# Performance work log

Hardware: AMD Instinct MI355X
Metric: run time of the kernel (lower is better)

Reference implementation:

```python
import jax, jax.numpy as jnp
import numpy as np

N_NODES = 100000
N_EDGES = 1600000
NFEAT = 64
NHID = 64
NCLASS = 40


def setup_inputs() -> dict:
    key = jax.random.key(0)
    ks = jax.random.split(key, 8)
    x = jax.random.normal(ks[0], (N_NODES, NFEAT), dtype=jnp.float32)
    edge_index = jax.random.randint(ks[1], (2, N_EDGES), 0, N_NODES, dtype=jnp.int64)
    # Kaiming-ish small init for Linear weights (stored as [in, out])
    def lin(k, fan_in, fan_out):
        bound = 1.0 / np.sqrt(fan_in)
        kw, kb = jax.random.split(k)
        W = jax.random.uniform(kw, (fan_in, fan_out), jnp.float32, -bound, bound)
        b = jax.random.uniform(kb, (fan_out,), jnp.float32, -bound, bound)
        return W, b
    W1, b1 = lin(ks[2], NFEAT, NHID)
    W2, b2 = lin(ks[3], NHID, NHID)
    Wf, bf = lin(ks[4], NHID, NCLASS)
    return {"x": x, "edge_index": edge_index, "W1": W1, "b1": b1,
            "W2": W2, "b2": b2, "Wf": Wf, "bf": bf}


def _gin_conv(h, src, dst, W, b, n_nodes):
    # PyG GINConv, eps=0: nn(x + sum_{j in N(i)} x_j), nn = Linear -> ReLU
    msg = h[src]                                   # [E, d] gather
    agg = jax.ops.segment_sum(msg, dst, num_segments=n_nodes)  # [N, d] scatter-add
    return jax.nn.relu((h + agg) @ W + b)


def reference(x, edge_index, W1, b1, W2, b2, Wf, bf):
    src, dst = edge_index[0], edge_index[1]
    n = x.shape[0]
    # layer 1: outer F.relu is idempotent on the ReLU inside GINConv's nn
    h = jax.nn.relu(_gin_conv(x, src, dst, W1, b1, n))
    # dropout is identity in eval mode
    h = jax.nn.relu(_gin_conv(h, src, dst, W2, b2, n))
    logits = h @ Wf + bf
    return jax.nn.log_softmax(logits, axis=1)
```

## Files before the change

### kernel.cpp

```cpp
#include <hip/hip_runtime.h>
#include <math.h>

#define N_NODES 100000
#define N_EDGES 1600000
#define NFEAT 64
#define NCLASS 40

#define SCAN_CHUNK 1024
#define SCAN_BLOCKS ((N_NODES + SCAN_CHUNK - 1) / SCAN_CHUNK)

#define NRANGES 8
#define RSZ ((N_NODES + NRANGES - 1) / NRANGES)
#define FILL_SLOTS 64

__device__ __forceinline__ float bf2f(unsigned short u) {
  return __uint_as_float(((unsigned int)u) << 16);
}
__device__ __forceinline__ unsigned short f2bf(float f) {
  unsigned int u = __float_as_uint(f);
  u += 0x7FFFu + ((u >> 16) & 1u);
  return (unsigned short)(u >> 16);
}

__global__ __launch_bounds__(256) void hist_rank_cvt_k(
    const int* __restrict__ dst, int* __restrict__ deg,
    unsigned short* __restrict__ rank, const float* __restrict__ x,
    unsigned short* __restrict__ xb) {
  int e = blockIdx.x * 256 + threadIdx.x;
  if (e < N_EDGES) {
    rank[e] = (unsigned short)atomicAdd(&deg[dst[e]], 1);
    float4 v = reinterpret_cast<const float4*>(x)[e];
    ushort4 o;
    o.x = f2bf(v.x); o.y = f2bf(v.y); o.z = f2bf(v.z); o.w = f2bf(v.w);
    reinterpret_cast<ushort4*>(xb)[e] = o;
  }
}

__global__ __launch_bounds__(256) void scan_partial_k(
    const int* __restrict__ deg, int* __restrict__ blockSums) {
  __shared__ int red[256];
  int b = blockIdx.x, t = threadIdx.x;
  int base = b * SCAN_CHUNK;
  int s = 0;
  for (int i = t; i < SCAN_CHUNK; i += 256) {
    int idx = base + i;
    if (idx < N_NODES) s += deg[idx];
  }
  red[t] = s;
  __syncthreads();
  for (int off = 128; off; off >>= 1) {
    if (t < off) red[t] += red[t + off];
    __syncthreads();
  }
  if (t == 0) blockSums[b] = red[0];
}

__global__ __launch_bounds__(128) void scan_sums_k(int* __restrict__ blockSums,
                                                   int* __restrict__ offs) {
  __shared__ int part[128];
  int t = threadIdx.x;
  int v = (t < SCAN_BLOCKS) ? blockSums[t] : 0;
  part[t] = v;
  __syncthreads();
  for (int off = 1; off < 128; off <<= 1) {
    int add = (t >= off) ? part[t - off] : 0;
    __syncthreads();
    part[t] += add;
    __syncthreads();
  }
  if (t < SCAN_BLOCKS) blockSums[t] = (t == 0) ? 0 : part[t - 1];
  if (t == 127) offs[N_NODES] = part[127];
}

__global__ __launch_bounds__(256) void scan_final_k(
    const int* __restrict__ deg, const int* __restrict__ blockOffs,
    int* __restrict__ offs) {
  __shared__ int part[256];
  int b = blockIdx.x, t = threadIdx.x;
  int base = b * SCAN_CHUNK + t * 4;
  int v0 = 0, v1 = 0, v2 = 0, v3 = 0;
  if (base + 3 < N_NODES) {
    v0 = deg[base]; v1 = deg[base + 1]; v2 = deg[base + 2]; v3 = deg[base + 3];
  } else {
    if (base + 0 < N_NODES) v0 = deg[base + 0];
    if (base + 1 < N_NODES) v1 = deg[base + 1];
    if (base + 2 < N_NODES) v2 = deg[base + 2];
    if (base + 3 < N_NODES) v3 = deg[base + 3];
  }
  part[t] = v0 + v1 + v2 + v3;
  __syncthreads();
  for (int off = 1; off < 256; off <<= 1) {
    int add = (t >= off) ? part[t - off] : 0;
    __syncthreads();
    part[t] += add;
    __syncthreads();
  }
  int run = blockOffs[b] + ((t == 0) ? 0 : part[t - 1]);
  if (base + 0 < N_NODES) { offs[base + 0] = run; run += v0; }
  if (base + 1 < N_NODES) { offs[base + 1] = run; run += v1; }
  if (base + 2 < N_NODES) { offs[base + 2] = run; run += v2; }
  if (base + 3 < N_NODES) { offs[base + 3] = run; run += v3; }
}

__global__ __launch_bounds__(256) void fill_csr_xcd_k(
    const int* __restrict__ src, const int* __restrict__ dst,
    const unsigned short* __restrict__ rank, const int* __restrict__ offs,
    int* __restrict__ csr) {
  const int NQ = N_EDGES / 4;
  int range = blockIdx.x & (NRANGES - 1);
  int slot = blockIdx.x >> 3;
  unsigned int lo = range * RSZ;

  for (int q = slot * 256 + threadIdx.x; q < NQ; q += FILL_SLOTS * 256) {
    int e = q << 2;
    int4 s = *reinterpret_cast<const int4*>(src + e);
    int4 d = *reinterpret_cast<const int4*>(dst + e);
    ushort4 r = *reinterpret_cast<const ushort4*>(rank + e);
    if ((unsigned int)(d.x - lo) < (unsigned int)RSZ) csr[offs[d.x] + r.x] = s.x;
    if ((unsigned int)(d.y - lo) < (unsigned int)RSZ) csr[offs[d.y] + r.y] = s.y;
    if ((unsigned int)(d.z - lo) < (unsigned int)RSZ) csr[offs[d.z] + r.z] = s.z;
    if ((unsigned int)(d.w - lo) < (unsigned int)RSZ) csr[offs[d.w] + r.w] = s.w;
  }
}

__global__ __launch_bounds__(256) void gather_b_k(
    const unsigned short* __restrict__ hb, const int* __restrict__ offs,
    const int* __restrict__ csr, unsigned short* __restrict__ aggb) {
  int t = threadIdx.x;
  int wv = t >> 6;
  int lane = t & 63;
  int g = lane >> 4;
  int l = lane & 15;
  int node = blockIdx.x * 4 + wv;
  if (node >= N_NODES) return;

  int beg = offs[node], end = offs[node + 1];
  float a0 = 0.f, a1 = 0.f, a2 = 0.f, a3 = 0.f;
  int e = beg + g;
  for (; e + 4 < end; e += 8) {
    int s0 = csr[e];
    int s1 = csr[e + 4];
    ushort4 u0 = *reinterpret_cast<const ushort4*>(hb + (size_t)s0 * NFEAT + (l << 2));
    ushort4 u1 = *reinterpret_cast<const ushort4*>(hb + (size_t)s1 * NFEAT + (l << 2));
    a0 += bf2f(u0.x) + bf2f(u1.x);
    a1 += bf2f(u0.y) + bf2f(u1.y);
    a2 += bf2f(u0.z) + bf2f(u1.z);
    a3 += bf2f(u0.w) + bf2f(u1.w);
  }
  if (e < end) {
    int s = csr[e];
    ushort4 u = *reinterpret_cast<const ushort4*>(hb + (size_t)s * NFEAT + (l << 2));
    a0 += bf2f(u.x); a1 += bf2f(u.y); a2 += bf2f(u.z); a3 += bf2f(u.w);
  }
  a0 += __shfl_xor(a0, 16); a1 += __shfl_xor(a1, 16);
  a2 += __shfl_xor(a2, 16); a3 += __shfl_xor(a3, 16);
  a0 += __shfl_xor(a0, 32); a1 += __shfl_xor(a1, 32);
  a2 += __shfl_xor(a2, 32); a3 += __shfl_xor(a3, 32);

  if (g == 0) {
    ushort4 u = *reinterpret_cast<const ushort4*>(hb + (size_t)node * NFEAT + (l << 2));
    ushort4 o;
    o.x = f2bf(a0 + bf2f(u.x)); o.y = f2bf(a1 + bf2f(u.y));
    o.z = f2bf(a2 + bf2f(u.z)); o.w = f2bf(a3 + bf2f(u.w));
    *reinterpret_cast<ushort4*>(aggb + (size_t)node * NFEAT + (l << 2)) = o;
  }
}

__global__ __launch_bounds__(256) void linear_relu_b_k(
    const unsigned short* __restrict__ inb, const float* __restrict__ W,
    const float* __restrict__ b, unsigned short* __restrict__ outb) {
  __shared__ float sIn[32][68];
  __shared__ float sWT[64][68];
  int r0 = blockIdx.x * 32;
  int t = threadIdx.x;
  for (int i = t; i < 64 * 64; i += 256) {
    int k = i >> 6, c = i & 63;
    sWT[c][k] = W[i];
  }
  for (int i = t; i < 512; i += 256) {
    int r = i >> 4, q = i & 15;
    ushort4 u = *reinterpret_cast<const ushort4*>(
        inb + (size_t)(r0 + r) * NFEAT + (q << 2));
    float4 v;
    v.x = bf2f(u.x); v.y = bf2f(u.y); v.z = bf2f(u.z); v.w = bf2f(u.w);
    *reinterpret_cast<float4*>(&sIn[r][q << 2]) = v;
  }
  __syncthreads();

  int c = t & 63;
  int rb = t >> 6;
  float acc[8];
#pragma unroll
  for (int i = 0; i < 8; ++i) acc[i] = 0.f;
#pragma unroll
  for (int kq = 0; kq < 16; ++kq) {
    float4 w = *reinterpret_cast<const float4*>(&sWT[c][kq << 2]);
#pragma unroll
    for (int i = 0; i < 8; ++i) {
      float4 v = *reinterpret_cast<const float4*>(&sIn[rb * 8 + i][kq << 2]);
      acc[i] = fmaf(v.x, w.x, fmaf(v.y, w.y, fmaf(v.z, w.z, fmaf(v.w, w.w, acc[i]))));
    }
  }
  float bias = b[c];
#pragma unroll
  for (int i = 0; i < 8; ++i) {
    int gr = r0 + rb * 8 + i;
    outb[(size_t)gr * NFEAT + c] = f2bf(fmaxf(acc[i] + bias, 0.f));
  }
}

__global__ __launch_bounds__(256) void fused_l2_final_k(
    const unsigned short* __restrict__ inb, const float* __restrict__ W2,
    const float* __restrict__ b2, const float* __restrict__ Wf,
    const float* __restrict__ bf, float* __restrict__ out) {
  __shared__ float sIn[32][68];
  __shared__ float sWT[64][68];
  __shared__ float sWfT[NCLASS][68];
  __shared__ float sH[32][68];
  __shared__ float sLse[32];
  float (*sLg)[41] = reinterpret_cast<float(*)[41]>(&sIn[0][0]);

  int r0 = blockIdx.x * 32;
  int t = threadIdx.x;
  int c = t & 63;
  int rb = t >> 6;

  for (int i = t; i < 64 * 64; i += 256) {
    int k = i >> 6, cc = i & 63;
    sWT[cc][k] = W2[i];
  }
  for (int i = t; i < 64 * NCLASS; i += 256) {
    int k = i / NCLASS, cc = i - k * NCLASS;
    sWfT[cc][k] = Wf[i];
  }
  for (int i = t; i < 512; i += 256) {
    int r = i >> 4, q = i & 15;
    ushort4 u = *reinterpret_cast<const ushort4*>(
        inb + (size_t)(r0 + r) * NFEAT + (q << 2));
    float4 v;
    v.x = bf2f(u.x); v.y = bf2f(u.y); v.z = bf2f(u.z); v.w = bf2f(u.w);
    *reinterpret_cast<float4*>(&sIn[r][q << 2]) = v;
  }
  __syncthreads();

  float acc[8];
#pragma unroll
  for (int i = 0; i < 8; ++i) acc[i] = 0.f;
#pragma unroll
  for (int kq = 0; kq < 16; ++kq) {
    float4 w = *reinterpret_cast<const float4*>(&sWT[c][kq << 2]);
#pragma unroll
    for (int i = 0; i < 8; ++i) {
      float4 v = *reinterpret_cast<const float4*>(&sIn[rb * 8 + i][kq << 2]);
      acc[i] = fmaf(v.x, w.x, fmaf(v.y, w.y, fmaf(v.z, w.z, fmaf(v.w, w.w, acc[i]))));
    }
  }
  float bias = b2[c];
#pragma unroll
  for (int i = 0; i < 8; ++i)
    sH[rb * 8 + i][c] = fmaxf(acc[i] + bias, 0.f);
  __syncthreads();

  if (c < NCLASS) {
    float lg[8];
    float bfc = bf[c];
#pragma unroll
    for (int i = 0; i < 8; ++i) lg[i] = bfc;
#pragma unroll
    for (int kq = 0; kq < 16; ++kq) {
      float4 w = *reinterpret_cast<const float4*>(&sWfT[c][kq << 2]);
#pragma unroll
      for (int i = 0; i < 8; ++i) {
        float4 v = *reinterpret_cast<const float4*>(&sH[rb * 8 + i][kq << 2]);
        lg[i] = fmaf(v.x, w.x, fmaf(v.y, w.y, fmaf(v.z, w.z, fmaf(v.w, w.w, lg[i]))));
      }
    }
#pragma unroll
    for (int i = 0; i < 8; ++i) sLg[rb * 8 + i][c] = lg[i];
  }
  __syncthreads();

  if (t < 32) {
    float m = -INFINITY;
#pragma unroll
    for (int j = 0; j < NCLASS; ++j) m = fmaxf(m, sLg[t][j]);
    float s = 0.f;
#pragma unroll
    for (int j = 0; j < NCLASS; ++j) s += expf(sLg[t][j] - m);
    sLse[t] = m + logf(s);
  }
  __syncthreads();

  for (int i = t; i < 32 * NCLASS; i += 256) {
    int r = i / NCLASS, cc = i - r * NCLASS;
    out[(size_t)(r0 + r) * NCLASS + cc] = sLg[r][cc] - sLse[r];
  }
}

extern "C" void kernel_launch(void* const* d_in, const int* in_sizes, int n_in,
                              void* d_out, int out_size, void* d_ws, size_t ws_size,
                              hipStream_t stream) {
  const float* x  = (const float*)d_in[0];
  const int*   ei = (const int*)d_in[1];
  const float* W1 = (const float*)d_in[2];
  const float* b1 = (const float*)d_in[3];
  const float* W2 = (const float*)d_in[4];
  const float* b2 = (const float*)d_in[5];
  const float* Wf = (const float*)d_in[6];
  const float* bf = (const float*)d_in[7];
  float* out = (float*)d_out;

  const int* src = ei;
  const int* dst = ei + N_EDGES;

  const size_t featElems = (size_t)N_NODES * NFEAT;
  unsigned short* xb   = (unsigned short*)d_ws;
  unsigned short* h1b  = xb + featElems;
  unsigned short* aggA = h1b + featElems;
  unsigned short* aggC = aggA + featElems;
  unsigned short* rank = aggC + featElems;
  int* deg       = (int*)(rank + N_EDGES);
  int* offs      = deg + N_NODES;
  int* blockSums = offs + N_NODES + 1;
  int* csr       = blockSums + 128;

  const int edgeBlocks   = (N_EDGES + 255) / 256;
  const int gatherBlocks = (N_NODES + 3) / 4;
  const int linBlocks    = (N_NODES + 31) / 32;

  hipMemsetAsync(deg, 0, N_NODES * sizeof(int), stream);
  hist_rank_cvt_k<<<edgeBlocks, 256, 0, stream>>>(dst, deg, rank, x, xb);
  scan_partial_k<<<SCAN_BLOCKS, 256, 0, stream>>>(deg, blockSums);
  scan_sums_k<<<1, 128, 0, stream>>>(blockSums, offs);
  scan_final_k<<<SCAN_BLOCKS, 256, 0, stream>>>(deg, blockSums, offs);
  fill_csr_xcd_k<<<NRANGES * FILL_SLOTS, 256, 0, stream>>>(src, dst, rank, offs, csr);

  gather_b_k<<<gatherBlocks, 256, 0, stream>>>(xb, offs, csr, aggA);
  linear_relu_b_k<<<linBlocks, 256, 0, stream>>>(aggA, W1, b1, h1b);

  gather_b_k<<<gatherBlocks, 256, 0, stream>>>(h1b, offs, csr, aggC);
  fused_l2_final_k<<<linBlocks, 256, 0, stream>>>(aggC, W2, b2, Wf, bf, out);
}
```

Baseline: 371.5 us.

## Split degree histogram into 8 sub-counters per node and unroll gather by four

Edge counting now spreads atomics over 8 sub-counters per destination node, selected by edge index mod 8, to reduce contention on same-address atomicAdds. The scan kernels read the 8 sub-counts and emit per-sub-bucket base offsets, which the CSR fill uses for placement. The gather loop is also unrolled to four neighbors in flight per lane group. In exchange the counter array and memset grow eightfold, the scan and fill read more data, and an extra base8 array is written.

```diff
diff --git a/kernel.cpp b/kernel.cpp
--- a/kernel.cpp
+++ b/kernel.cpp
@@ -23,12 +23,13 @@
 }
 
 __global__ __launch_bounds__(256) void hist_rank_cvt_k(
-    const int* __restrict__ dst, int* __restrict__ deg,
-    unsigned short* __restrict__ rank, const float* __restrict__ x,
+    const int* __restrict__ dst, int* __restrict__ cnt8,
+    unsigned short* __restrict__ subrank, const float* __restrict__ x,
     unsigned short* __restrict__ xb) {
   int e = blockIdx.x * 256 + threadIdx.x;
   if (e < N_EDGES) {
-    rank[e] = (unsigned short)atomicAdd(&deg[dst[e]], 1);
+    int d = dst[e];
+    subrank[e] = (unsigned short)atomicAdd(&cnt8[(d << 3) | (e & 7)], 1);
     float4 v = reinterpret_cast<const float4*>(x)[e];
     ushort4 o;
     o.x = f2bf(v.x); o.y = f2bf(v.y); o.z = f2bf(v.z); o.w = f2bf(v.w);
@@ -37,14 +38,18 @@
 }
 
 __global__ __launch_bounds__(256) void scan_partial_k(
-    const int* __restrict__ deg, int* __restrict__ blockSums) {
+    const int* __restrict__ cnt8, int* __restrict__ blockSums) {
   __shared__ int red[256];
   int b = blockIdx.x, t = threadIdx.x;
   int base = b * SCAN_CHUNK;
   int s = 0;
   for (int i = t; i < SCAN_CHUNK; i += 256) {
     int idx = base + i;
-    if (idx < N_NODES) s += deg[idx];
+    if (idx < N_NODES) {
+      const int4* p = reinterpret_cast<const int4*>(cnt8 + ((size_t)idx << 3));
+      int4 a = p[0], c = p[1];
+      s += a.x + a.y + a.z + a.w + c.x + c.y + c.z + c.w;
+    }
   }
   red[t] = s;
   __syncthreads();
@@ -73,21 +78,27 @@
 }
 
 __global__ __launch_bounds__(256) void scan_final_k(
-    const int* __restrict__ deg, const int* __restrict__ blockOffs,
-    int* __restrict__ offs) {
+    const int* __restrict__ cnt8, const int* __restrict__ blockOffs,
+    int* __restrict__ offs, int* __restrict__ base8) {
   __shared__ int part[256];
   int b = blockIdx.x, t = threadIdx.x;
   int base = b * SCAN_CHUNK + t * 4;
-  int v0 = 0, v1 = 0, v2 = 0, v3 = 0;
-  if (base + 3 < N_NODES) {
-    v0 = deg[base]; v1 = deg[base + 1]; v2 = deg[base + 2]; v3 = deg[base + 3];
-  } else {
-    if (base + 0 < N_NODES) v0 = deg[base + 0];
-    if (base + 1 < N_NODES) v1 = deg[base + 1];
-    if (base + 2 < N_NODES) v2 = deg[base + 2];
-    if (base + 3 < N_NODES) v3 = deg[base + 3];
-  }
-  part[t] = v0 + v1 + v2 + v3;
+  int c8[4][8];
+  int tot[4];
+#pragma unroll
+  for (int k = 0; k < 4; ++k) {
+    int n = base + k;
+    tot[k] = 0;
+    if (n < N_NODES) {
+      const int4* p = reinterpret_cast<const int4*>(cnt8 + ((size_t)n << 3));
+      int4 a = p[0], c = p[1];
+      c8[k][0] = a.x; c8[k][1] = a.y; c8[k][2] = a.z; c8[k][3] = a.w;
+      c8[k][4] = c.x; c8[k][5] = c.y; c8[k][6] = c.z; c8[k][7] = c.w;
+#pragma unroll
+      for (int j = 0; j < 8; ++j) tot[k] += c8[k][j];
+    }
+  }
+  part[t] = tot[0] + tot[1] + tot[2] + tot[3];
   __syncthreads();
   for (int off = 1; off < 256; off <<= 1) {
     int add = (t >= off) ? part[t - off] : 0;
@@ -96,15 +107,26 @@
     __syncthreads();
   }
   int run = blockOffs[b] + ((t == 0) ? 0 : part[t - 1]);
-  if (base + 0 < N_NODES) { offs[base + 0] = run; run += v0; }
-  if (base + 1 < N_NODES) { offs[base + 1] = run; run += v1; }
-  if (base + 2 < N_NODES) { offs[base + 2] = run; run += v2; }
-  if (base + 3 < N_NODES) { offs[base + 3] = run; run += v3; }
+#pragma unroll
+  for (int k = 0; k < 4; ++k) {
+    int n = base + k;
+    if (n < N_NODES) {
+      offs[n] = run;
+      int pref = run;
+      int bb[8];
+#pragma unroll
+      for (int j = 0; j < 8; ++j) { bb[j] = pref; pref += c8[k][j]; }
+      int4* q = reinterpret_cast<int4*>(base8 + ((size_t)n << 3));
+      q[0] = make_int4(bb[0], bb[1], bb[2], bb[3]);
+      q[1] = make_int4(bb[4], bb[5], bb[6], bb[7]);
+      run += tot[k];
+    }
+  }
 }
 
 __global__ __launch_bounds__(256) void fill_csr_xcd_k(
     const int* __restrict__ src, const int* __restrict__ dst,
-    const unsigned short* __restrict__ rank, const int* __restrict__ offs,
+    const unsigned short* __restrict__ subrank, const int* __restrict__ base8,
     int* __restrict__ csr) {
   const int NQ = N_EDGES / 4;
   int range = blockIdx.x & (NRANGES - 1);
@@ -115,11 +137,15 @@
     int e = q << 2;
     int4 s = *reinterpret_cast<const int4*>(src + e);
     int4 d = *reinterpret_cast<const int4*>(dst + e);
-    ushort4 r = *reinterpret_cast<const ushort4*>(rank + e);
-    if ((unsigned int)(d.x - lo) < (unsigned int)RSZ) csr[offs[d.x] + r.x] = s.x;
-    if ((unsigned int)(d.y - lo) < (unsigned int)RSZ) csr[offs[d.y] + r.y] = s.y;
-    if ((unsigned int)(d.z - lo) < (unsigned int)RSZ) csr[offs[d.z] + r.z] = s.z;
-    if ((unsigned int)(d.w - lo) < (unsigned int)RSZ) csr[offs[d.w] + r.w] = s.w;
+    ushort4 r = *reinterpret_cast<const ushort4*>(subrank + e);
+    if ((unsigned int)(d.x - lo) < (unsigned int)RSZ)
+      csr[base8[(d.x << 3) | ((e + 0) & 7)] + r.x] = s.x;
+    if ((unsigned int)(d.y - lo) < (unsigned int)RSZ)
+      csr[base8[(d.y << 3) | ((e + 1) & 7)] + r.y] = s.y;
+    if ((unsigned int)(d.z - lo) < (unsigned int)RSZ)
+      csr[base8[(d.z << 3) | ((e + 2) & 7)] + r.z] = s.z;
+    if ((unsigned int)(d.w - lo) < (unsigned int)RSZ)
+      csr[base8[(d.w << 3) | ((e + 3) & 7)] + r.w] = s.w;
   }
 }
 
@@ -137,17 +163,21 @@
   int beg = offs[node], end = offs[node + 1];
   float a0 = 0.f, a1 = 0.f, a2 = 0.f, a3 = 0.f;
   int e = beg + g;
-  for (; e + 4 < end; e += 8) {
+  for (; e + 12 < end; e += 16) {
     int s0 = csr[e];
     int s1 = csr[e + 4];
+    int s2 = csr[e + 8];
+    int s3 = csr[e + 12];
     ushort4 u0 = *reinterpret_cast<const ushort4*>(hb + (size_t)s0 * NFEAT + (l << 2));
     ushort4 u1 = *reinterpret_cast<const ushort4*>(hb + (size_t)s1 * NFEAT + (l << 2));
-    a0 += bf2f(u0.x) + bf2f(u1.x);
-    a1 += bf2f(u0.y) + bf2f(u1.y);
-    a2 += bf2f(u0.z) + bf2f(u1.z);
-    a3 += bf2f(u0.w) + bf2f(u1.w);
-  }
-  if (e < end) {
+    ushort4 u2 = *reinterpret_cast<const ushort4*>(hb + (size_t)s2 * NFEAT + (l << 2));
+    ushort4 u3 = *reinterpret_cast<const ushort4*>(hb + (size_t)s3 * NFEAT + (l << 2));
+    a0 += (bf2f(u0.x) + bf2f(u1.x)) + (bf2f(u2.x) + bf2f(u3.x));
+    a1 += (bf2f(u0.y) + bf2f(u1.y)) + (bf2f(u2.y) + bf2f(u3.y));
+    a2 += (bf2f(u0.z) + bf2f(u1.z)) + (bf2f(u2.z) + bf2f(u3.z));
+    a3 += (bf2f(u0.w) + bf2f(u1.w)) + (bf2f(u2.w) + bf2f(u3.w));
+  }
+  for (; e < end; e += 4) {
     int s = csr[e];
     ushort4 u = *reinterpret_cast<const ushort4*>(hb + (size_t)s * NFEAT + (l << 2));
     a0 += bf2f(u.x); a1 += bf2f(u.y); a2 += bf2f(u.z); a3 += bf2f(u.w);
@@ -318,9 +348,10 @@
   unsigned short* h1b  = xb + featElems;
   unsigned short* aggA = h1b + featElems;
   unsigned short* aggC = aggA + featElems;
-  unsigned short* rank = aggC + featElems;
-  int* deg       = (int*)(rank + N_EDGES);
-  int* offs      = deg + N_NODES;
+  unsigned short* subrank = aggC + featElems;
+  int* cnt8      = (int*)(subrank + N_EDGES);
+  int* base8     = cnt8 + (size_t)N_NODES * 8;
+  int* offs      = base8 + (size_t)N_NODES * 8;
   int* blockSums = offs + N_NODES + 1;
   int* csr       = blockSums + 128;
 
@@ -328,12 +359,12 @@
   const int gatherBlocks = (N_NODES + 3) / 4;
   const int linBlocks    = (N_NODES + 31) / 32;
 
-  hipMemsetAsync(deg, 0, N_NODES * sizeof(int), stream);
-  hist_rank_cvt_k<<<edgeBlocks, 256, 0, stream>>>(dst, deg, rank, x, xb);
-  scan_partial_k<<<SCAN_BLOCKS, 256, 0, stream>>>(deg, blockSums);
+  hipMemsetAsync(cnt8, 0, (size_t)N_NODES * 8 * sizeof(int), stream);
+  hist_rank_cvt_k<<<edgeBlocks, 256, 0, stream>>>(dst, cnt8, subrank, x, xb);
+  scan_partial_k<<<SCAN_BLOCKS, 256, 0, stream>>>(cnt8, blockSums);
   scan_sums_k<<<1, 128, 0, stream>>>(blockSums, offs);
-  scan_final_k<<<SCAN_BLOCKS, 256, 0, stream>>>(deg, blockSums, offs);
-  fill_csr_xcd_k<<<NRANGES * FILL_SLOTS, 256, 0, stream>>>(src, dst, rank, offs, csr);
+  scan_final_k<<<SCAN_BLOCKS, 256, 0, stream>>>(cnt8, blockSums, offs, base8);
+  fill_csr_xcd_k<<<NRANGES * FILL_SLOTS, 256, 0, stream>>>(src, dst, subrank, base8, csr);
 
   gather_b_k<<<gatherBlocks, 256, 0, stream>>>(xb, offs, csr, aggA);
   linear_relu_b_k<<<linBlocks, 256, 0, stream>>>(aggA, W1, b1, h1b);
```

Measured after the change: 382.3 us. +2.9%, slower.

## Build CSR with LDS-privatized per-slot histograms instead of global atomics

Applied to the files above, without the earlier changes.

Replaces the global-atomic degree histogram and per-edge rank array with per-block LDS histograms over node ranges and edge stripes. A slot-scan kernel then turns these into per-slot base offsets, and the fill kernel uses LDS atomics to place edges. This removes 1.6M contended global atomics and the rank buffer, at the cost of a 12.5k-int LDS array per block, a new scan kernel and extra slotCnt traffic. The gather loop is also unrolled to four edges per group so more loads are in flight.

```diff
diff --git a/kernel.cpp b/kernel.cpp
--- a/kernel.cpp
+++ b/kernel.cpp
@@ -10,8 +10,12 @@
 #define SCAN_BLOCKS ((N_NODES + SCAN_CHUNK - 1) / SCAN_CHUNK)
 
 #define NRANGES 8
-#define RSZ ((N_NODES + NRANGES - 1) / NRANGES)
-#define FILL_SLOTS 64
+#define RSZ (N_NODES / NRANGES)
+#define NSLOTS 32
+#define NQ (N_EDGES / 4)
+#define NFQ (N_NODES * NFEAT / 4)
+#define QSTRIPE (NQ / NSLOTS)
+#define SLOT_STRIDE 12512
 
 __device__ __forceinline__ float bf2f(unsigned short u) {
   return __uint_as_float(((unsigned int)u) << 16);
@@ -22,17 +26,71 @@
   return (unsigned short)(u >> 16);
 }
 
-__global__ __launch_bounds__(256) void hist_rank_cvt_k(
-    const int* __restrict__ dst, int* __restrict__ deg,
-    unsigned short* __restrict__ rank, const float* __restrict__ x,
-    unsigned short* __restrict__ xb) {
-  int e = blockIdx.x * 256 + threadIdx.x;
-  if (e < N_EDGES) {
-    rank[e] = (unsigned short)atomicAdd(&deg[dst[e]], 1);
-    float4 v = reinterpret_cast<const float4*>(x)[e];
+__global__ __launch_bounds__(256) void hist_lds_k(
+    const int* __restrict__ dst, int* __restrict__ slotCnt,
+    const float* __restrict__ x, unsigned short* __restrict__ xb) {
+  __shared__ int cnt[RSZ];
+  int t = threadIdx.x;
+  int r = blockIdx.x & (NRANGES - 1);
+  int s = blockIdx.x >> 3;
+  unsigned int lo = r * RSZ;
+
+  for (int i = t; i < RSZ; i += 256) cnt[i] = 0;
+
+  for (int g = blockIdx.x * 256 + t; g < NFQ; g += 256 * 256) {
+    float4 v = reinterpret_cast<const float4*>(x)[g];
     ushort4 o;
     o.x = f2bf(v.x); o.y = f2bf(v.y); o.z = f2bf(v.z); o.w = f2bf(v.w);
-    reinterpret_cast<ushort4*>(xb)[e] = o;
+    reinterpret_cast<ushort4*>(xb)[g] = o;
+  }
+  __syncthreads();
+
+  int q0 = s * QSTRIPE;
+  for (int q = q0 + t; q < q0 + QSTRIPE; q += 256) {
+    int4 d = *reinterpret_cast<const int4*>(dst + (q << 2));
+    unsigned int a;
+    a = d.x - lo; if (a < (unsigned int)RSZ) atomicAdd(&cnt[a], 1);
+    a = d.y - lo; if (a < (unsigned int)RSZ) atomicAdd(&cnt[a], 1);
+    a = d.z - lo; if (a < (unsigned int)RSZ) atomicAdd(&cnt[a], 1);
+    a = d.w - lo; if (a < (unsigned int)RSZ) atomicAdd(&cnt[a], 1);
+  }
+  __syncthreads();
+
+  int* dstRow = slotCnt + (size_t)(s * NRANGES + r) * SLOT_STRIDE;
+  for (int i = t; i < RSZ; i += 256) dstRow[i] = cnt[i];
+}
+
+__global__ __launch_bounds__(256) void slot_scan_k(int* __restrict__ slotCnt,
+                                                   int* __restrict__ deg) {
+  __shared__ int tile[NSLOTS][257];
+  const int CHUNKS = (RSZ + 255) / 256;
+  int t = threadIdx.x;
+  int r = blockIdx.x / CHUNKS;
+  int chunk = blockIdx.x % CHUNKS;
+  int L = chunk * 256 + t;
+  bool ok = (L < RSZ);
+
+  for (int s = 0; s < NSLOTS; ++s) {
+    int v = 0;
+    if (ok) v = slotCnt[(size_t)(s * NRANGES + r) * SLOT_STRIDE + L];
+    tile[s][t] = v;
+  }
+  __syncthreads();
+
+  if (ok) {
+    int run = 0;
+#pragma unroll
+    for (int s = 0; s < NSLOTS; ++s) {
+      int v = tile[s][t];
+      tile[s][t] = run;
+      run += v;
+    }
+    deg[r * RSZ + L] = run;
+  }
+  __syncthreads();
+
+  for (int s = 0; s < NSLOTS; ++s) {
+    if (ok) slotCnt[(size_t)(s * NRANGES + r) * SLOT_STRIDE + L] = tile[s][t];
   }
 }
 
@@ -102,24 +160,46 @@
   if (base + 3 < N_NODES) { offs[base + 3] = run; run += v3; }
 }
 
-__global__ __launch_bounds__(256) void fill_csr_xcd_k(
+__global__ __launch_bounds__(256) void fill_lds_k(
     const int* __restrict__ src, const int* __restrict__ dst,
-    const unsigned short* __restrict__ rank, const int* __restrict__ offs,
+    const int* __restrict__ slotBase, const int* __restrict__ offs,
     int* __restrict__ csr) {
-  const int NQ = N_EDGES / 4;
-  int range = blockIdx.x & (NRANGES - 1);
-  int slot = blockIdx.x >> 3;
-  unsigned int lo = range * RSZ;
-
-  for (int q = slot * 256 + threadIdx.x; q < NQ; q += FILL_SLOTS * 256) {
+  __shared__ int cur[RSZ];
+  int t = threadIdx.x;
+  int r = blockIdx.x & (NRANGES - 1);
+  int s = blockIdx.x >> 3;
+  unsigned int lo = r * RSZ;
+
+  for (int i = t; i < RSZ; i += 256) cur[i] = 0;
+  __syncthreads();
+
+  const int* baseRow = slotBase + (size_t)(s * NRANGES + r) * SLOT_STRIDE;
+  int q0 = s * QSTRIPE;
+  for (int q = q0 + t; q < q0 + QSTRIPE; q += 256) {
     int e = q << 2;
-    int4 s = *reinterpret_cast<const int4*>(src + e);
-    int4 d = *reinterpret_cast<const int4*>(dst + e);
-    ushort4 r = *reinterpret_cast<const ushort4*>(rank + e);
-    if ((unsigned int)(d.x - lo) < (unsigned int)RSZ) csr[offs[d.x] + r.x] = s.x;
-    if ((unsigned int)(d.y - lo) < (unsigned int)RSZ) csr[offs[d.y] + r.y] = s.y;
-    if ((unsigned int)(d.z - lo) < (unsigned int)RSZ) csr[offs[d.z] + r.z] = s.z;
-    if ((unsigned int)(d.w - lo) < (unsigned int)RSZ) csr[offs[d.w] + r.w] = s.w;
+    int4 d4 = *reinterpret_cast<const int4*>(dst + e);
+    int4 s4 = *reinterpret_cast<const int4*>(src + e);
+    unsigned int a;
+    a = d4.x - lo;
+    if (a < (unsigned int)RSZ) {
+      int p = atomicAdd(&cur[a], 1);
+      csr[offs[d4.x] + baseRow[a] + p] = s4.x;
+    }
+    a = d4.y - lo;
+    if (a < (unsigned int)RSZ) {
+      int p = atomicAdd(&cur[a], 1);
+      csr[offs[d4.y] + baseRow[a] + p] = s4.y;
+    }
+    a = d4.z - lo;
+    if (a < (unsigned int)RSZ) {
+      int p = atomicAdd(&cur[a], 1);
+      csr[offs[d4.z] + baseRow[a] + p] = s4.z;
+    }
+    a = d4.w - lo;
+    if (a < (unsigned int)RSZ) {
+      int p = atomicAdd(&cur[a], 1);
+      csr[offs[d4.w] + baseRow[a] + p] = s4.w;
+    }
   }
 }
 
@@ -137,17 +217,21 @@
   int beg = offs[node], end = offs[node + 1];
   float a0 = 0.f, a1 = 0.f, a2 = 0.f, a3 = 0.f;
   int e = beg + g;
-  for (; e + 4 < end; e += 8) {
+  for (; e + 12 < end; e += 16) {
     int s0 = csr[e];
     int s1 = csr[e + 4];
+    int s2 = csr[e + 8];
+    int s3 = csr[e + 12];
     ushort4 u0 = *reinterpret_cast<const ushort4*>(hb + (size_t)s0 * NFEAT + (l << 2));
     ushort4 u1 = *reinterpret_cast<const ushort4*>(hb + (size_t)s1 * NFEAT + (l << 2));
-    a0 += bf2f(u0.x) + bf2f(u1.x);
-    a1 += bf2f(u0.y) + bf2f(u1.y);
-    a2 += bf2f(u0.z) + bf2f(u1.z);
-    a3 += bf2f(u0.w) + bf2f(u1.w);
-  }
-  if (e < end) {
+    ushort4 u2 = *reinterpret_cast<const ushort4*>(hb + (size_t)s2 * NFEAT + (l << 2));
+    ushort4 u3 = *reinterpret_cast<const ushort4*>(hb + (size_t)s3 * NFEAT + (l << 2));
+    a0 += (bf2f(u0.x) + bf2f(u1.x)) + (bf2f(u2.x) + bf2f(u3.x));
+    a1 += (bf2f(u0.y) + bf2f(u1.y)) + (bf2f(u2.y) + bf2f(u3.y));
+    a2 += (bf2f(u0.z) + bf2f(u1.z)) + (bf2f(u2.z) + bf2f(u3.z));
+    a3 += (bf2f(u0.w) + bf2f(u1.w)) + (bf2f(u2.w) + bf2f(u3.w));
+  }
+  for (; e < end; e += 4) {
     int s = csr[e];
     ushort4 u = *reinterpret_cast<const ushort4*>(hb + (size_t)s * NFEAT + (l << 2));
     a0 += bf2f(u.x); a1 += bf2f(u.y); a2 += bf2f(u.z); a3 += bf2f(u.w);
@@ -318,22 +402,23 @@
   unsigned short* h1b  = xb + featElems;
   unsigned short* aggA = h1b + featElems;
   unsigned short* aggC = aggA + featElems;
-  unsigned short* rank = aggC + featElems;
-  int* deg       = (int*)(rank + N_EDGES);
+  int* slotCnt   = (int*)(aggC + featElems);
+  int* deg       = slotCnt + (size_t)NSLOTS * NRANGES * SLOT_STRIDE;
   int* offs      = deg + N_NODES;
   int* blockSums = offs + N_NODES + 1;
   int* csr       = blockSums + 128;
 
-  const int edgeBlocks   = (N_EDGES + 255) / 256;
+  const int histBlocks   = NRANGES * NSLOTS;
+  const int s1Blocks     = NRANGES * ((RSZ + 255) / 256);
   const int gatherBlocks = (N_NODES + 3) / 4;
   const int linBlocks    = (N_NODES + 31) / 32;
 
-  hipMemsetAsync(deg, 0, N_NODES * sizeof(int), stream);
-  hist_rank_cvt_k<<<edgeBlocks, 256, 0, stream>>>(dst, deg, rank, x, xb);
+  hist_lds_k<<<histBlocks, 256, 0, stream>>>(dst, slotCnt, x, xb);
+  slot_scan_k<<<s1Blocks, 256, 0, stream>>>(slotCnt, deg);
   scan_partial_k<<<SCAN_BLOCKS, 256, 0, stream>>>(deg, blockSums);
   scan_sums_k<<<1, 128, 0, stream>>>(blockSums, offs);
   scan_final_k<<<SCAN_BLOCKS, 256, 0, stream>>>(deg, blockSums, offs);
-  fill_csr_xcd_k<<<NRANGES * FILL_SLOTS, 256, 0, stream>>>(src, dst, rank, offs, csr);
+  fill_lds_k<<<histBlocks, 256, 0, stream>>>(src, dst, slotCnt, offs, csr);
 
   gather_b_k<<<gatherBlocks, 256, 0, stream>>>(xb, offs, csr, aggA);
   linear_relu_b_k<<<linBlocks, 256, 0, stream>>>(aggA, W1, b1, h1b);
```

After: 404.5 us. +8.9%, slower.

## Split node features into 16-wide column chunks for cache-friendly gathers

Applied to the files above, without the earlier changes.

Feature matrices are stored as four column chunks of 16 bf16 values per node, so each chunk occupies 3.2MB. The gather kernel runs one pass per chunk, with blocks ordered chunk-major, so that the randomly accessed working set is more likely to fit in L2/LLC. Each wavefront now walks 16 edges in parallel, with 4 lanes covering one 32-byte row, and reduces the partial sums with extra shuffles. The cost is that the csr and offs arrays are read four times and each gather request is only 32 bytes.

```diff
diff --git a/kernel.cpp b/kernel.cpp
--- a/kernel.cpp
+++ b/kernel.cpp
@@ -13,6 +13,10 @@
 #define RSZ ((N_NODES + NRANGES - 1) / NRANGES)
 #define FILL_SLOTS 64
 
+#define CHUNKS 4
+#define CF 16
+#define NODE_GRPS ((N_NODES + 3) / 4)
+
 __device__ __forceinline__ float bf2f(unsigned short u) {
   return __uint_as_float(((unsigned int)u) << 16);
 }
@@ -25,14 +29,16 @@
 __global__ __launch_bounds__(256) void hist_rank_cvt_k(
     const int* __restrict__ dst, int* __restrict__ deg,
     unsigned short* __restrict__ rank, const float* __restrict__ x,
-    unsigned short* __restrict__ xb) {
+    unsigned short* __restrict__ xbc) {
   int e = blockIdx.x * 256 + threadIdx.x;
   if (e < N_EDGES) {
     rank[e] = (unsigned short)atomicAdd(&deg[dst[e]], 1);
     float4 v = reinterpret_cast<const float4*>(x)[e];
     ushort4 o;
     o.x = f2bf(v.x); o.y = f2bf(v.y); o.z = f2bf(v.z); o.w = f2bf(v.w);
-    reinterpret_cast<ushort4*>(xb)[e] = o;
+    int row = e >> 4, q = e & 15;
+    reinterpret_cast<ushort4*>(xbc)[(size_t)(q >> 2) * N_NODES * 4 +
+                                    (size_t)row * 4 + (q & 3)] = o;
   }
 }
 
@@ -123,46 +129,44 @@
   }
 }
 
-__global__ __launch_bounds__(256) void gather_b_k(
-    const unsigned short* __restrict__ hb, const int* __restrict__ offs,
-    const int* __restrict__ csr, unsigned short* __restrict__ aggb) {
+__global__ __launch_bounds__(256) void gather_chunk_k(
+    const unsigned short* __restrict__ hbc, const int* __restrict__ offs,
+    const int* __restrict__ csr, unsigned short* __restrict__ aggc) {
+  int grp = blockIdx.x % NODE_GRPS;
+  int chunk = blockIdx.x / NODE_GRPS;
   int t = threadIdx.x;
   int wv = t >> 6;
   int lane = t & 63;
-  int g = lane >> 4;
-  int l = lane & 15;
-  int node = blockIdx.x * 4 + wv;
+  int g = lane >> 2;
+  int l = lane & 3;
+  int node = grp * 4 + wv;
   if (node >= N_NODES) return;
+
+  const unsigned short* hb = hbc + (size_t)chunk * N_NODES * CF;
+  unsigned short* ag = aggc + (size_t)chunk * N_NODES * CF;
 
   int beg = offs[node], end = offs[node + 1];
   float a0 = 0.f, a1 = 0.f, a2 = 0.f, a3 = 0.f;
-  int e = beg + g;
-  for (; e + 4 < end; e += 8) {
-    int s0 = csr[e];
-    int s1 = csr[e + 4];
-    ushort4 u0 = *reinterpret_cast<const ushort4*>(hb + (size_t)s0 * NFEAT + (l << 2));
-    ushort4 u1 = *reinterpret_cast<const ushort4*>(hb + (size_t)s1 * NFEAT + (l << 2));
-    a0 += bf2f(u0.x) + bf2f(u1.x);
-    a1 += bf2f(u0.y) + bf2f(u1.y);
-    a2 += bf2f(u0.z) + bf2f(u1.z);
-    a3 += bf2f(u0.w) + bf2f(u1.w);
-  }
-  if (e < end) {
+  for (int e = beg + g; e < end; e += 16) {
     int s = csr[e];
-    ushort4 u = *reinterpret_cast<const ushort4*>(hb + (size_t)s * NFEAT + (l << 2));
+    ushort4 u = *reinterpret_cast<const ushort4*>(hb + (size_t)s * CF + (l << 2));
     a0 += bf2f(u.x); a1 += bf2f(u.y); a2 += bf2f(u.z); a3 += bf2f(u.w);
   }
+  a0 += __shfl_xor(a0, 4);  a1 += __shfl_xor(a1, 4);
+  a2 += __shfl_xor(a2, 4);  a3 += __shfl_xor(a3, 4);
+  a0 += __shfl_xor(a0, 8);  a1 += __shfl_xor(a1, 8);
+  a2 += __shfl_xor(a2, 8);  a3 += __shfl_xor(a3, 8);
   a0 += __shfl_xor(a0, 16); a1 += __shfl_xor(a1, 16);
   a2 += __shfl_xor(a2, 16); a3 += __shfl_xor(a3, 16);
   a0 += __shfl_xor(a0, 32); a1 += __shfl_xor(a1, 32);
   a2 += __shfl_xor(a2, 32); a3 += __shfl_xor(a3, 32);
 
   if (g == 0) {
-    ushort4 u = *reinterpret_cast<const ushort4*>(hb + (size_t)node * NFEAT + (l << 2));
+    ushort4 u = *reinterpret_cast<const ushort4*>(hb + (size_t)node * CF + (l << 2));
     ushort4 o;
     o.x = f2bf(a0 + bf2f(u.x)); o.y = f2bf(a1 + bf2f(u.y));
     o.z = f2bf(a2 + bf2f(u.z)); o.w = f2bf(a3 + bf2f(u.w));
-    *reinterpret_cast<ushort4*>(aggb + (size_t)node * NFEAT + (l << 2)) = o;
+    *reinterpret_cast<ushort4*>(ag + (size_t)node * CF + (l << 2)) = o;
   }
 }
 
@@ -179,8 +183,8 @@
   }
   for (int i = t; i < 512; i += 256) {
     int r = i >> 4, q = i & 15;
-    ushort4 u = *reinterpret_cast<const ushort4*>(
-        inb + (size_t)(r0 + r) * NFEAT + (q << 2));
+    ushort4 u = reinterpret_cast<const ushort4*>(inb)[
+        (size_t)(q >> 2) * N_NODES * 4 + (size_t)(r0 + r) * 4 + (q & 3)];
     float4 v;
     v.x = bf2f(u.x); v.y = bf2f(u.y); v.z = bf2f(u.z); v.w = bf2f(u.w);
     *reinterpret_cast<float4*>(&sIn[r][q << 2]) = v;
@@ -202,10 +206,12 @@
     }
   }
   float bias = b[c];
+  int chc = c >> 4, f = c & 15;
 #pragma unroll
   for (int i = 0; i < 8; ++i) {
     int gr = r0 + rb * 8 + i;
-    outb[(size_t)gr * NFEAT + c] = f2bf(fmaxf(acc[i] + bias, 0.f));
+    outb[(size_t)chc * N_NODES * CF + (size_t)gr * CF + f] =
+        f2bf(fmaxf(acc[i] + bias, 0.f));
   }
 }
 
@@ -235,8 +241,8 @@
   }
   for (int i = t; i < 512; i += 256) {
     int r = i >> 4, q = i & 15;
-    ushort4 u = *reinterpret_cast<const ushort4*>(
-        inb + (size_t)(r0 + r) * NFEAT + (q << 2));
+    ushort4 u = reinterpret_cast<const ushort4*>(inb)[
+        (size_t)(q >> 2) * N_NODES * 4 + (size_t)(r0 + r) * 4 + (q & 3)];
     float4 v;
     v.x = bf2f(u.x); v.y = bf2f(u.y); v.z = bf2f(u.z); v.w = bf2f(u.w);
     *reinterpret_cast<float4*>(&sIn[r][q << 2]) = v;
@@ -314,9 +320,9 @@
   const int* dst = ei + N_EDGES;
 
   const size_t featElems = (size_t)N_NODES * NFEAT;
-  unsigned short* xb   = (unsigned short*)d_ws;
-  unsigned short* h1b  = xb + featElems;
-  unsigned short* aggA = h1b + featElems;
+  unsigned short* xbc  = (unsigned short*)d_ws;
+  unsigned short* h1bc = xbc + featElems;
+  unsigned short* aggA = h1bc + featElems;
   unsigned short* aggC = aggA + featElems;
   unsigned short* rank = aggC + featElems;
   int* deg       = (int*)(rank + N_EDGES);
@@ -325,19 +331,19 @@
   int* csr       = blockSums + 128;
 
   const int edgeBlocks   = (N_EDGES + 255) / 256;
-  const int gatherBlocks = (N_NODES + 3) / 4;
+  const int gatherBlocks = CHUNKS * NODE_GRPS;
   const int linBlocks    = (N_NODES + 31) / 32;
 
   hipMemsetAsync(deg, 0, N_NODES * sizeof(int), stream);
-  hist_rank_cvt_k<<<edgeBlocks, 256, 0, stream>>>(dst, deg, rank, x, xb);
+  hist_rank_cvt_k<<<edgeBlocks, 256, 0, stream>>>(dst, deg, rank, x, xbc);
   scan_partial_k<<<SCAN_BLOCKS, 256, 0, stream>>>(deg, blockSums);
   scan_sums_k<<<1, 128, 0, stream>>>(blockSums, offs);
   scan_final_k<<<SCAN_BLOCKS, 256, 0, stream>>>(deg, blockSums, offs);
   fill_csr_xcd_k<<<NRANGES * FILL_SLOTS, 256, 0, stream>>>(src, dst, rank, offs, csr);
 
-  gather_b_k<<<gatherBlocks, 256, 0, stream>>>(xb, offs, csr, aggA);
-  linear_relu_b_k<<<linBlocks, 256, 0, stream>>>(aggA, W1, b1, h1b);
-
-  gather_b_k<<<gatherBlocks, 256, 0, stream>>>(h1b, offs, csr, aggC);
+  gather_chunk_k<<<gatherBlocks, 256, 0, stream>>>(xbc, offs, csr, aggA);
+  linear_relu_b_k<<<linBlocks, 256, 0, stream>>>(aggA, W1, b1, h1bc);
+
+  gather_chunk_k<<<gatherBlocks, 256, 0, stream>>>(h1bc, offs, csr, aggC);
   fused_l2_final_k<<<linBlocks, 256, 0, stream>>>(aggC, W2, b2, Wf, bf, out);
 }
```

New measurement: 500.1 us. 1.35x slower.
